# Kernel tuning notes

Hardware: AMD Instinct MI355X
Metric: run time of the kernel (lower is better)

Reference implementation:

```python
import jax, jax.numpy as jnp
import numpy as np

BETA_MEM = 0.9
BETA_INH = 0.6
THRESHOLD = 1.0
SURR_ALPHA = 2.0  # snntorch default ATan surrogate alpha


@jax.custom_vjp
def spike_fn(x):
    # Heaviside spike with ATan surrogate gradient (snntorch default).
    return (x > 0).astype(x.dtype)


def _spike_fwd(x):
    return spike_fn(x), x


def _spike_bwd(x, g):
    # d/dx ATan surrogate: alpha/2 / (1 + (pi/2 * alpha * x)^2); alpha=2 -> 1/(1+(pi*x)^2)
    pi_half_alpha = jnp.float32(np.pi / 2.0 * SURR_ALPHA)
    grad = (SURR_ALPHA / 2.0) / (1.0 + (pi_half_alpha * x) ** 2)
    return (g * grad.astype(x.dtype),)


spike_fn.defvjp(_spike_fwd, _spike_bwd)


def setup_inputs() -> dict:
    key = jax.random.key(0)
    k1, = jax.random.split(key, 1)
    T, B = 4096, 4096
    # Bernoulli(0.05) spike trains on the two input channels (FM1, FM3)
    spike_seq = (jax.random.uniform(k1, (T, B, 2)) < 0.05).astype(jnp.float32)
    # fc_exc weight pinned to [[0, 1]] in the original module
    w_exc = jnp.array([[0.0, 1.0]], dtype=jnp.float32)
    # inhibitory weight parameter initialized to 0.0
    w_inh = jnp.float32(0.0)
    return {"spike_seq": spike_seq, "w_exc": w_exc, "w_inh": w_inh}


def reference(spike_seq, w_exc, w_inh):
    T, B, _ = spike_seq.shape
    mem0 = jnp.zeros((B, 1), dtype=spike_seq.dtype)
    inh0 = jnp.zeros((B, 1), dtype=spike_seq.dtype)

    def step(carry, x_t):
        mem, inh_state = carry
        cur_exc = x_t @ w_exc.T                       # [B,1]
        fm1_t = x_t[:, 0:1]                           # [B,1]
        inh_state = BETA_INH * inh_state + fm1_t
        cur_inh = w_inh * inh_state
        cur = cur_exc + cur_inh
        # snntorch Leaky (reset-by-subtraction): reset uses spike of PREVIOUS mem
        reset = spike_fn(mem - THRESHOLD)
        mem_new = BETA_MEM * mem + cur - reset * THRESHOLD
        spk = spike_fn(mem_new - THRESHOLD)
        return (mem_new, inh_state), (spk, cur_exc, cur_inh, mem_new)

    _, (spk_rec, exc_rec, inh_rec, mem_rec) = jax.lax.scan(step, (mem0, inh0), spike_seq)
    return spk_rec, exc_rec, inh_rec, mem_rec
```

## Files before the change

kernel.cpp:

```cpp
#include <hip/hip_runtime.h>
#include <stdint.h>

#define T_STEPS 4096
#define B_SIZE  4096
#define NWORDS  (T_STEPS / 32)
#define B2      (B_SIZE / 2)
#define B4      (B_SIZE / 4)


__device__ __forceinline__ float bitf(uint32_t w, int k) {
    return (float)((w >> k) & 1u);
}

__global__ __launch_bounds__(256) void k_pack(const float4* __restrict__ x,
                                              uint2* __restrict__ p0,
                                              uint2* __restrict__ p1) {
    uint32_t gid = blockIdx.x * 256u + threadIdx.x;
    uint32_t i  = gid >> 11;
    uint32_t bp = gid & (B2 - 1);
    const float4* xp = x + (size_t)i * 32u * B2 + bp;
    uint32_t e0 = 0u, e1 = 0u, o0 = 0u, o1 = 0u;
#pragma unroll
    for (int k = 0; k < 32; ++k) {
        float4 v = xp[(size_t)k * B2];
        e0 |= ((uint32_t)(v.x != 0.0f)) << k;
        e1 |= ((uint32_t)(v.y != 0.0f)) << k;
        o0 |= ((uint32_t)(v.z != 0.0f)) << k;
        o1 |= ((uint32_t)(v.w != 0.0f)) << k;
    }
    p0[(size_t)i * B2 + bp] = make_uint2(e0, o0);
    p1[(size_t)i * B2 + bp] = make_uint2(e1, o1);
}

__global__ __launch_bounds__(256) void k_scan(const uint32_t* __restrict__ p0,
                                              const uint32_t* __restrict__ p1,
                                              const float* __restrict__ w_exc,
                                              const float* __restrict__ w_inh_p,
                                              float* __restrict__ mem_ck,
                                              float* __restrict__ inh_ck) {
    int b = blockIdx.x * 256 + threadIdx.x;
    const float w00 = w_exc[0], w01 = w_exc[1], winh = w_inh_p[0];
    float mem = 0.0f, inh = 0.0f;

    if (w00 == 0.0f && winh == 0.0f) {
        uint32_t w1 = p1[b];
        for (int i = 0; i < NWORDS; ++i) {
            uint32_t w1n = (i + 1 < NWORDS) ? p1[(size_t)(i + 1) * B_SIZE + b] : 0u;
            mem_ck[(size_t)i * B_SIZE + b] = mem;
#pragma unroll
            for (int k = 0; k < 32; ++k) {
                float x1f = bitf(w1, k);
                float r   = (mem > 1.0f) ? 1.0f : 0.0f;
                float m1  = __fmul_rn(0.9f, mem);
                float m2  = __fmaf_rn(x1f, w01, m1);
                mem       = __fsub_rn(m2, r);
            }
            w1 = w1n;
        }
    } else {
        uint32_t w0 = p0[b], w1 = p1[b];
        for (int i = 0; i < NWORDS; ++i) {
            uint32_t w0n = (i + 1 < NWORDS) ? p0[(size_t)(i + 1) * B_SIZE + b] : 0u;
            uint32_t w1n = (i + 1 < NWORDS) ? p1[(size_t)(i + 1) * B_SIZE + b] : 0u;
            mem_ck[(size_t)i * B_SIZE + b] = mem;
            inh_ck[(size_t)i * B_SIZE + b] = inh;
#pragma unroll
            for (int k = 0; k < 32; ++k) {
                float x0f = bitf(w0, k);
                float x1f = bitf(w1, k);
                float exc = __fadd_rn(__fmul_rn(x0f, w00), __fmul_rn(x1f, w01));
                inh       = __fadd_rn(__fmul_rn(0.6f, inh), x0f);
                float ci  = __fmul_rn(winh, inh);
                float cur = __fadd_rn(exc, ci);
                float r   = (mem > 1.0f) ? 1.0f : 0.0f;
                float m1  = __fmul_rn(0.9f, mem);
                float m2  = __fadd_rn(m1, cur);
                mem       = __fsub_rn(m2, r);
            }
            w0 = w0n; w1 = w1n;
        }
    }
}

__global__ __launch_bounds__(256) void k_replay(const uint32_t* __restrict__ p0,
                                                const uint32_t* __restrict__ p1,
                                                const float* __restrict__ w_exc,
                                                const float* __restrict__ w_inh_p,
                                                const float* __restrict__ mem_ck,
                                                const float* __restrict__ inh_ck,
                                                float* __restrict__ out) {
    uint32_t gid = blockIdx.x * 256u + threadIdx.x;
    uint32_t i = gid >> 10;
    uint32_t q = gid & (B4 - 1);
    float4* __restrict__ spk4 = (float4*)out;
    float4* __restrict__ exc4 = (float4*)(out + (size_t)T_STEPS * B_SIZE);
    float4* __restrict__ inh4 = (float4*)(out + 2 * (size_t)T_STEPS * B_SIZE);
    float4* __restrict__ mem4 = (float4*)(out + 3 * (size_t)T_STEPS * B_SIZE);
    const float w00 = w_exc[0], w01 = w_exc[1], winh = w_inh_p[0];

    float4 mem = ((const float4*)mem_ck)[(size_t)i * B4 + q];
    uint4  w1q = ((const uint4*)p1)[(size_t)i * B4 + q];
    size_t base = (size_t)i * 32u * B4 + q;

    if (w00 == 0.0f && winh == 0.0f) {
        const float4 z4 = make_float4(0.0f, 0.0f, 0.0f, 0.0f);
#pragma unroll
        for (int k = 0; k < 32; ++k) {
            float4 x1f = make_float4(bitf(w1q.x, k), bitf(w1q.y, k),
                                     bitf(w1q.z, k), bitf(w1q.w, k));
            float4 exc, spk;
            {
                float r = (mem.x > 1.0f) ? 1.0f : 0.0f;
                exc.x = __fmul_rn(x1f.x, w01);
                mem.x = __fsub_rn(__fmaf_rn(x1f.x, w01, __fmul_rn(0.9f, mem.x)), r);
                spk.x = (mem.x > 1.0f) ? 1.0f : 0.0f;
            }
            {
                float r = (mem.y > 1.0f) ? 1.0f : 0.0f;
                exc.y = __fmul_rn(x1f.y, w01);
                mem.y = __fsub_rn(__fmaf_rn(x1f.y, w01, __fmul_rn(0.9f, mem.y)), r);
                spk.y = (mem.y > 1.0f) ? 1.0f : 0.0f;
            }
            {
                float r = (mem.z > 1.0f) ? 1.0f : 0.0f;
                exc.z = __fmul_rn(x1f.z, w01);
                mem.z = __fsub_rn(__fmaf_rn(x1f.z, w01, __fmul_rn(0.9f, mem.z)), r);
                spk.z = (mem.z > 1.0f) ? 1.0f : 0.0f;
            }
            {
                float r = (mem.w > 1.0f) ? 1.0f : 0.0f;
                exc.w = __fmul_rn(x1f.w, w01);
                mem.w = __fsub_rn(__fmaf_rn(x1f.w, w01, __fmul_rn(0.9f, mem.w)), r);
                spk.w = (mem.w > 1.0f) ? 1.0f : 0.0f;
            }
            size_t idx = base + (size_t)k * B4;
            spk4[idx] = spk;
            exc4[idx] = exc;
            inh4[idx] = z4;
            mem4[idx] = mem;
        }
    } else {
        float4 inh = ((const float4*)inh_ck)[(size_t)i * B4 + q];
        uint4  w0q = ((const uint4*)p0)[(size_t)i * B4 + q];
#pragma unroll
        for (int k = 0; k < 32; ++k) {
            float4 excv, civ, spkv;
#define STEP(C)                                                              \
            {                                                                \
                float x0f = bitf(w0q.C, k);                                  \
                float x1f = bitf(w1q.C, k);                                  \
                float exc = __fadd_rn(__fmul_rn(x0f, w00), __fmul_rn(x1f, w01)); \
                inh.C     = __fadd_rn(__fmul_rn(0.6f, inh.C), x0f);          \
                float ci  = __fmul_rn(winh, inh.C);                          \
                float cur = __fadd_rn(exc, ci);                              \
                float r   = (mem.C > 1.0f) ? 1.0f : 0.0f;                    \
                mem.C     = __fsub_rn(__fadd_rn(__fmul_rn(0.9f, mem.C), cur), r); \
                excv.C = exc; civ.C = ci;                                    \
                spkv.C = (mem.C > 1.0f) ? 1.0f : 0.0f;                       \
            }
            STEP(x) STEP(y) STEP(z) STEP(w)
#undef STEP
            size_t idx = base + (size_t)k * B4;
            spk4[idx] = spkv;
            exc4[idx] = excv;
            inh4[idx] = civ;
            mem4[idx] = mem;
        }
    }
}

__global__ __launch_bounds__(256) void k_naive(const float2* __restrict__ x,
                                               const float* __restrict__ w_exc,
                                               const float* __restrict__ w_inh_p,
                                               float* __restrict__ out) {
    int b = blockIdx.x * 256 + threadIdx.x;
    const float w00 = w_exc[0], w01 = w_exc[1], winh = w_inh_p[0];
    float* __restrict__ spk_o = out;
    float* __restrict__ exc_o = out + (size_t)T_STEPS * B_SIZE;
    float* __restrict__ inh_o = out + 2 * (size_t)T_STEPS * B_SIZE;
    float* __restrict__ mem_o = out + 3 * (size_t)T_STEPS * B_SIZE;
    float mem = 0.0f, inh = 0.0f;
    for (int t = 0; t < T_STEPS; ++t) {
        float2 v = x[(size_t)t * B_SIZE + b];
        float exc = __fadd_rn(__fmul_rn(v.x, w00), __fmul_rn(v.y, w01));
        inh       = __fadd_rn(__fmul_rn(0.6f, inh), v.x);
        float ci  = __fmul_rn(winh, inh);
        float cur = __fadd_rn(exc, ci);
        float r   = (mem > 1.0f) ? 1.0f : 0.0f;
        float m1  = __fmul_rn(0.9f, mem);
        mem       = __fsub_rn(__fadd_rn(m1, cur), r);
        float spk = (mem > 1.0f) ? 1.0f : 0.0f;
        size_t idx = (size_t)t * B_SIZE + b;
        spk_o[idx] = spk; exc_o[idx] = exc; inh_o[idx] = ci; mem_o[idx] = mem;
    }
}

extern "C" void kernel_launch(void* const* d_in, const int* in_sizes, int n_in,
                              void* d_out, int out_size, void* d_ws, size_t ws_size,
                              hipStream_t stream) {
    const float4* x4     = (const float4*)d_in[0];
    const float*  w_exc  = (const float*)d_in[1];
    const float*  w_inh  = (const float*)d_in[2];
    float* out = (float*)d_out;

    const size_t nw = (size_t)NWORDS * B_SIZE;
    const size_t need = nw * (sizeof(uint32_t) * 2 + sizeof(float) * 2);

    if (ws_size >= need) {
        uint32_t* p0     = (uint32_t*)d_ws;
        uint32_t* p1     = p0 + nw;
        float*    mem_ck = (float*)(p1 + nw);
        float*    inh_ck = mem_ck + nw;

        k_pack<<<(NWORDS * B2) / 256, 256, 0, stream>>>(x4, (uint2*)p0, (uint2*)p1);
        k_scan<<<B_SIZE / 256, 256, 0, stream>>>(p0, p1, w_exc, w_inh, mem_ck, inh_ck);
        k_replay<<<(NWORDS * B4) / 256, 256, 0, stream>>>(p0, p1, w_exc, w_inh,
                                                          mem_ck, inh_ck, out);
    } else {
        k_naive<<<B_SIZE / 256, 256, 0, stream>>>((const float2*)d_in[0], w_exc, w_inh, out);
    }
}
```

Measured before the change: 434.2 us.

## Use nontemporal loads/stores, deeper scan prefetch, and smaller scan blocks

The pack kernel now reads the input with nontemporal loads, and the replay kernel writes all four output streams with nontemporal stores, so streaming traffic does not pollute the cache. The serial scan kernel prefetches four packed words per iteration instead of one to hide load latency. It also launches 64-thread blocks instead of 256, spreading the 4096 sequential lanes over more compute units. This trades some register use and code size for more latency hiding and wider spread of the latency-bound scan.

```diff
diff --git a/kernel.cpp b/kernel.cpp
--- a/kernel.cpp
+++ b/kernel.cpp
@@ -7,77 +7,121 @@
 #define B2      (B_SIZE / 2)
 #define B4      (B_SIZE / 4)
 
+typedef float    f32x4 __attribute__((ext_vector_type(4)));
+typedef uint32_t u32x4 __attribute__((ext_vector_type(4)));
+typedef uint32_t u32x2 __attribute__((ext_vector_type(2)));
+
 
 __device__ __forceinline__ float bitf(uint32_t w, int k) {
     return (float)((w >> k) & 1u);
 }
 
-__global__ __launch_bounds__(256) void k_pack(const float4* __restrict__ x,
-                                              uint2* __restrict__ p0,
-                                              uint2* __restrict__ p1) {
+__global__ __launch_bounds__(256) void k_pack(const f32x4* __restrict__ x,
+                                              u32x2* __restrict__ p0,
+                                              u32x2* __restrict__ p1) {
     uint32_t gid = blockIdx.x * 256u + threadIdx.x;
     uint32_t i  = gid >> 11;
     uint32_t bp = gid & (B2 - 1);
-    const float4* xp = x + (size_t)i * 32u * B2 + bp;
+    const f32x4* xp = x + (size_t)i * 32u * B2 + bp;
     uint32_t e0 = 0u, e1 = 0u, o0 = 0u, o1 = 0u;
 #pragma unroll
     for (int k = 0; k < 32; ++k) {
-        float4 v = xp[(size_t)k * B2];
+        f32x4 v = __builtin_nontemporal_load(xp + (size_t)k * B2);
         e0 |= ((uint32_t)(v.x != 0.0f)) << k;
         e1 |= ((uint32_t)(v.y != 0.0f)) << k;
         o0 |= ((uint32_t)(v.z != 0.0f)) << k;
         o1 |= ((uint32_t)(v.w != 0.0f)) << k;
     }
-    p0[(size_t)i * B2 + bp] = make_uint2(e0, o0);
-    p1[(size_t)i * B2 + bp] = make_uint2(e1, o1);
-}
-
-__global__ __launch_bounds__(256) void k_scan(const uint32_t* __restrict__ p0,
-                                              const uint32_t* __restrict__ p1,
-                                              const float* __restrict__ w_exc,
-                                              const float* __restrict__ w_inh_p,
-                                              float* __restrict__ mem_ck,
-                                              float* __restrict__ inh_ck) {
-    int b = blockIdx.x * 256 + threadIdx.x;
+    u32x2 s0; s0.x = e0; s0.y = o0;
+    u32x2 s1; s1.x = e1; s1.y = o1;
+    p0[(size_t)i * B2 + bp] = s0;
+    p1[(size_t)i * B2 + bp] = s1;
+}
+
+__global__ __launch_bounds__(64) void k_scan(const uint32_t* __restrict__ p0,
+                                             const uint32_t* __restrict__ p1,
+                                             const float* __restrict__ w_exc,
+                                             const float* __restrict__ w_inh_p,
+                                             float* __restrict__ mem_ck,
+                                             float* __restrict__ inh_ck) {
+    int b = blockIdx.x * 64 + threadIdx.x;
     const float w00 = w_exc[0], w01 = w_exc[1], winh = w_inh_p[0];
     float mem = 0.0f, inh = 0.0f;
 
     if (w00 == 0.0f && winh == 0.0f) {
-        uint32_t w1 = p1[b];
-        for (int i = 0; i < NWORDS; ++i) {
-            uint32_t w1n = (i + 1 < NWORDS) ? p1[(size_t)(i + 1) * B_SIZE + b] : 0u;
-            mem_ck[(size_t)i * B_SIZE + b] = mem;
-#pragma unroll
-            for (int k = 0; k < 32; ++k) {
-                float x1f = bitf(w1, k);
-                float r   = (mem > 1.0f) ? 1.0f : 0.0f;
-                float m1  = __fmul_rn(0.9f, mem);
-                float m2  = __fmaf_rn(x1f, w01, m1);
-                mem       = __fsub_rn(m2, r);
-            }
-            w1 = w1n;
+        uint32_t c0 = p1[b];
+        uint32_t c1 = p1[(size_t)1 * B_SIZE + b];
+        uint32_t c2 = p1[(size_t)2 * B_SIZE + b];
+        uint32_t c3 = p1[(size_t)3 * B_SIZE + b];
+        for (int i = 0; i < NWORDS; i += 4) {
+            uint32_t n0 = 0u, n1 = 0u, n2 = 0u, n3 = 0u;
+            if (i + 4 < NWORDS) {
+                n0 = p1[(size_t)(i + 4) * B_SIZE + b];
+                n1 = p1[(size_t)(i + 5) * B_SIZE + b];
+                n2 = p1[(size_t)(i + 6) * B_SIZE + b];
+                n3 = p1[(size_t)(i + 7) * B_SIZE + b];
+            }
+            uint32_t ws[4] = {c0, c1, c2, c3};
+#pragma unroll
+            for (int j = 0; j < 4; ++j) {
+                mem_ck[(size_t)(i + j) * B_SIZE + b] = mem;
+                uint32_t w1 = ws[j];
+#pragma unroll
+                for (int k = 0; k < 32; ++k) {
+                    float x1f = bitf(w1, k);
+                    float r   = (mem > 1.0f) ? 1.0f : 0.0f;
+                    float m1  = __fmul_rn(0.9f, mem);
+                    float m2  = __fmaf_rn(x1f, w01, m1);
+                    mem       = __fsub_rn(m2, r);
+                }
+            }
+            c0 = n0; c1 = n1; c2 = n2; c3 = n3;
         }
     } else {
-        uint32_t w0 = p0[b], w1 = p1[b];
-        for (int i = 0; i < NWORDS; ++i) {
-            uint32_t w0n = (i + 1 < NWORDS) ? p0[(size_t)(i + 1) * B_SIZE + b] : 0u;
-            uint32_t w1n = (i + 1 < NWORDS) ? p1[(size_t)(i + 1) * B_SIZE + b] : 0u;
-            mem_ck[(size_t)i * B_SIZE + b] = mem;
-            inh_ck[(size_t)i * B_SIZE + b] = inh;
-#pragma unroll
-            for (int k = 0; k < 32; ++k) {
-                float x0f = bitf(w0, k);
-                float x1f = bitf(w1, k);
-                float exc = __fadd_rn(__fmul_rn(x0f, w00), __fmul_rn(x1f, w01));
-                inh       = __fadd_rn(__fmul_rn(0.6f, inh), x0f);
-                float ci  = __fmul_rn(winh, inh);
-                float cur = __fadd_rn(exc, ci);
-                float r   = (mem > 1.0f) ? 1.0f : 0.0f;
-                float m1  = __fmul_rn(0.9f, mem);
-                float m2  = __fadd_rn(m1, cur);
-                mem       = __fsub_rn(m2, r);
-            }
-            w0 = w0n; w1 = w1n;
+        uint32_t a0 = p0[b];
+        uint32_t a1 = p0[(size_t)1 * B_SIZE + b];
+        uint32_t a2 = p0[(size_t)2 * B_SIZE + b];
+        uint32_t a3 = p0[(size_t)3 * B_SIZE + b];
+        uint32_t c0 = p1[b];
+        uint32_t c1 = p1[(size_t)1 * B_SIZE + b];
+        uint32_t c2 = p1[(size_t)2 * B_SIZE + b];
+        uint32_t c3 = p1[(size_t)3 * B_SIZE + b];
+        for (int i = 0; i < NWORDS; i += 4) {
+            uint32_t m0 = 0u, m1_ = 0u, m2_ = 0u, m3 = 0u;
+            uint32_t n0 = 0u, n1 = 0u, n2 = 0u, n3 = 0u;
+            if (i + 4 < NWORDS) {
+                m0 = p0[(size_t)(i + 4) * B_SIZE + b];
+                m1_ = p0[(size_t)(i + 5) * B_SIZE + b];
+                m2_ = p0[(size_t)(i + 6) * B_SIZE + b];
+                m3 = p0[(size_t)(i + 7) * B_SIZE + b];
+                n0 = p1[(size_t)(i + 4) * B_SIZE + b];
+                n1 = p1[(size_t)(i + 5) * B_SIZE + b];
+                n2 = p1[(size_t)(i + 6) * B_SIZE + b];
+                n3 = p1[(size_t)(i + 7) * B_SIZE + b];
+            }
+            uint32_t wa[4] = {a0, a1, a2, a3};
+            uint32_t wc[4] = {c0, c1, c2, c3};
+#pragma unroll
+            for (int j = 0; j < 4; ++j) {
+                mem_ck[(size_t)(i + j) * B_SIZE + b] = mem;
+                inh_ck[(size_t)(i + j) * B_SIZE + b] = inh;
+                uint32_t w0 = wa[j], w1 = wc[j];
+#pragma unroll
+                for (int k = 0; k < 32; ++k) {
+                    float x0f = bitf(w0, k);
+                    float x1f = bitf(w1, k);
+                    float exc = __fadd_rn(__fmul_rn(x0f, w00), __fmul_rn(x1f, w01));
+                    inh       = __fadd_rn(__fmul_rn(0.6f, inh), x0f);
+                    float ci  = __fmul_rn(winh, inh);
+                    float cur = __fadd_rn(exc, ci);
+                    float r   = (mem > 1.0f) ? 1.0f : 0.0f;
+                    float mm1 = __fmul_rn(0.9f, mem);
+                    float mm2 = __fadd_rn(mm1, cur);
+                    mem       = __fsub_rn(mm2, r);
+                }
+            }
+            a0 = m0; a1 = m1_; a2 = m2_; a3 = m3;
+            c0 = n0; c1 = n1; c2 = n2; c3 = n3;
         }
     }
 }
@@ -92,59 +136,43 @@
     uint32_t gid = blockIdx.x * 256u + threadIdx.x;
     uint32_t i = gid >> 10;
     uint32_t q = gid & (B4 - 1);
-    float4* __restrict__ spk4 = (float4*)out;
-    float4* __restrict__ exc4 = (float4*)(out + (size_t)T_STEPS * B_SIZE);
-    float4* __restrict__ inh4 = (float4*)(out + 2 * (size_t)T_STEPS * B_SIZE);
-    float4* __restrict__ mem4 = (float4*)(out + 3 * (size_t)T_STEPS * B_SIZE);
+    f32x4* __restrict__ spk4 = (f32x4*)out;
+    f32x4* __restrict__ exc4 = (f32x4*)(out + (size_t)T_STEPS * B_SIZE);
+    f32x4* __restrict__ inh4 = (f32x4*)(out + 2 * (size_t)T_STEPS * B_SIZE);
+    f32x4* __restrict__ mem4 = (f32x4*)(out + 3 * (size_t)T_STEPS * B_SIZE);
     const float w00 = w_exc[0], w01 = w_exc[1], winh = w_inh_p[0];
 
-    float4 mem = ((const float4*)mem_ck)[(size_t)i * B4 + q];
-    uint4  w1q = ((const uint4*)p1)[(size_t)i * B4 + q];
+    f32x4 mem = ((const f32x4*)mem_ck)[(size_t)i * B4 + q];
+    u32x4 w1q = ((const u32x4*)p1)[(size_t)i * B4 + q];
     size_t base = (size_t)i * 32u * B4 + q;
 
     if (w00 == 0.0f && winh == 0.0f) {
-        const float4 z4 = make_float4(0.0f, 0.0f, 0.0f, 0.0f);
+        f32x4 z4; z4.x = 0.0f; z4.y = 0.0f; z4.z = 0.0f; z4.w = 0.0f;
 #pragma unroll
         for (int k = 0; k < 32; ++k) {
-            float4 x1f = make_float4(bitf(w1q.x, k), bitf(w1q.y, k),
-                                     bitf(w1q.z, k), bitf(w1q.w, k));
-            float4 exc, spk;
-            {
-                float r = (mem.x > 1.0f) ? 1.0f : 0.0f;
-                exc.x = __fmul_rn(x1f.x, w01);
-                mem.x = __fsub_rn(__fmaf_rn(x1f.x, w01, __fmul_rn(0.9f, mem.x)), r);
-                spk.x = (mem.x > 1.0f) ? 1.0f : 0.0f;
-            }
-            {
-                float r = (mem.y > 1.0f) ? 1.0f : 0.0f;
-                exc.y = __fmul_rn(x1f.y, w01);
-                mem.y = __fsub_rn(__fmaf_rn(x1f.y, w01, __fmul_rn(0.9f, mem.y)), r);
-                spk.y = (mem.y > 1.0f) ? 1.0f : 0.0f;
-            }
-            {
-                float r = (mem.z > 1.0f) ? 1.0f : 0.0f;
-                exc.z = __fmul_rn(x1f.z, w01);
-                mem.z = __fsub_rn(__fmaf_rn(x1f.z, w01, __fmul_rn(0.9f, mem.z)), r);
-                spk.z = (mem.z > 1.0f) ? 1.0f : 0.0f;
-            }
-            {
-                float r = (mem.w > 1.0f) ? 1.0f : 0.0f;
-                exc.w = __fmul_rn(x1f.w, w01);
-                mem.w = __fsub_rn(__fmaf_rn(x1f.w, w01, __fmul_rn(0.9f, mem.w)), r);
-                spk.w = (mem.w > 1.0f) ? 1.0f : 0.0f;
-            }
+            f32x4 exc, spk;
+#define STEPF(C, W)                                                          \
+            {                                                                \
+                float x1f = bitf(W, k);                                      \
+                float r   = (mem.C > 1.0f) ? 1.0f : 0.0f;                    \
+                exc.C = __fmul_rn(x1f, w01);                                 \
+                mem.C = __fsub_rn(__fmaf_rn(x1f, w01, __fmul_rn(0.9f, mem.C)), r); \
+                spk.C = (mem.C > 1.0f) ? 1.0f : 0.0f;                        \
+            }
+            STEPF(x, w1q.x) STEPF(y, w1q.y) STEPF(z, w1q.z) STEPF(w, w1q.w)
+#undef STEPF
             size_t idx = base + (size_t)k * B4;
-            spk4[idx] = spk;
-            exc4[idx] = exc;
-            inh4[idx] = z4;
-            mem4[idx] = mem;
+            __builtin_nontemporal_store(spk, spk4 + idx);
+            __builtin_nontemporal_store(exc, exc4 + idx);
+            __builtin_nontemporal_store(z4,  inh4 + idx);
+            __builtin_nontemporal_store(mem, mem4 + idx);
         }
     } else {
-        float4 inh = ((const float4*)inh_ck)[(size_t)i * B4 + q];
-        uint4  w0q = ((const uint4*)p0)[(size_t)i * B4 + q];
+        f32x4 inh = ((const f32x4*)inh_ck)[(size_t)i * B4 + q];
+        u32x4 w0q = ((const u32x4*)p0)[(size_t)i * B4 + q];
 #pragma unroll
         for (int k = 0; k < 32; ++k) {
-            float4 excv, civ, spkv;
+            f32x4 excv, civ, spkv;
 #define STEP(C)                                                              \
             {                                                                \
                 float x0f = bitf(w0q.C, k);                                  \
@@ -161,10 +189,10 @@
             STEP(x) STEP(y) STEP(z) STEP(w)
 #undef STEP
             size_t idx = base + (size_t)k * B4;
-            spk4[idx] = spkv;
-            exc4[idx] = excv;
-            inh4[idx] = civ;
-            mem4[idx] = mem;
+            __builtin_nontemporal_store(spkv, spk4 + idx);
+            __builtin_nontemporal_store(excv, exc4 + idx);
+            __builtin_nontemporal_store(civ,  inh4 + idx);
+            __builtin_nontemporal_store(mem,  mem4 + idx);
         }
     }
 }
@@ -198,7 +226,7 @@
 extern "C" void kernel_launch(void* const* d_in, const int* in_sizes, int n_in,
                               void* d_out, int out_size, void* d_ws, size_t ws_size,
                               hipStream_t stream) {
-    const float4* x4     = (const float4*)d_in[0];
+    const f32x4*  x4     = (const f32x4*)d_in[0];
     const float*  w_exc  = (const float*)d_in[1];
     const float*  w_inh  = (const float*)d_in[2];
     float* out = (float*)d_out;
@@ -212,8 +240,8 @@
         float*    mem_ck = (float*)(p1 + nw);
         float*    inh_ck = mem_ck + nw;
 
-        k_pack<<<(NWORDS * B2) / 256, 256, 0, stream>>>(x4, (uint2*)p0, (uint2*)p1);
-        k_scan<<<B_SIZE / 256, 256, 0, stream>>>(p0, p1, w_exc, w_inh, mem_ck, inh_ck);
+        k_pack<<<(NWORDS * B2) / 256, 256, 0, stream>>>(x4, (u32x2*)p0, (u32x2*)p1);
+        k_scan<<<B_SIZE / 64, 64, 0, stream>>>(p0, p1, w_exc, w_inh, mem_ck, inh_ck);
         k_replay<<<(NWORDS * B4) / 256, 256, 0, stream>>>(p0, p1, w_exc, w_inh,
                                                           mem_ck, inh_ck, out);
     } else {
```

Result: no change. 432.4 us (-0.4%).
